# Kernel tuning notes

Measured on AMD Instinct MI355X. Metric: run time of the kernel, lower is better.

## Reference

```python
import jax, jax.numpy as jnp
import numpy as np

EPS = 1e-5


def setup_inputs() -> dict:
    key = jax.random.key(0)
    k_x, k_y, k_w, k_b = jax.random.split(key, 4)
    B, IN, OUT = 16384, 1024, 1024
    x = jax.random.normal(k_x, (B, IN), dtype=jnp.float32)
    y = jax.random.normal(k_y, (B, OUT), dtype=jnp.float32)
    # nn.Linear default init scale ~ 1/sqrt(in_features); keep activations sane
    weight = jax.random.normal(k_w, (OUT, IN), dtype=jnp.float32) / np.sqrt(IN)
    bias = jax.random.normal(k_b, (OUT,), dtype=jnp.float32) / np.sqrt(IN)
    gamma = jnp.ones((OUT,), dtype=jnp.float32)
    beta = jnp.zeros((OUT,), dtype=jnp.float32)
    return {"x": x, "y": y, "weight": weight, "bias": bias, "gamma": gamma, "beta": beta}


def reference(x, y, weight, bias, gamma, beta):
    # Linear: z[b, o] = sum_i x[b, i] * weight[o, i] + bias[o]
    z = jnp.einsum('bi,oi->bo', x, weight) + bias
    # LayerNorm over the feature (out_features) dim, biased variance
    mean = jnp.mean(z, axis=-1, keepdims=True)
    var = jnp.mean(jnp.square(z), axis=-1, keepdims=True) - jnp.square(mean)
    ln = (z - mean) * jax.lax.rsqrt(var + EPS) * gamma + beta
    # residual add then elementwise multiply
    return (ln + y) * y
```

## Files before the change

### kernel.cpp

```cpp
#include <hip/hip_runtime.h>
#include <stdint.h>

typedef unsigned short u16;
typedef __attribute__((ext_vector_type(8))) short short8;
typedef __attribute__((ext_vector_type(4))) float floatx4;
typedef __attribute__((ext_vector_type(2))) float floatx2;

#define K_DIM 1024
#define N_DIM 1024
#define BM 64
#define BK 32
#define NCHUNK (K_DIM / BK)

__device__ __forceinline__ u16 f2b(float f) {
    union { float f; uint32_t i; } v; v.f = f;
    uint32_t u = v.i;
    return (u16)((u + 0x7FFFu + ((u >> 16) & 1u)) >> 16);
}
__device__ __forceinline__ float b2f(u16 u) {
    union { uint32_t i; float f; } v; v.i = ((uint32_t)u) << 16; return v.f;
}

__global__ __launch_bounds__(256) void pack_w_kernel(const float* __restrict__ w,
                                                     u16* __restrict__ wpk) {
    int gid  = blockIdx.x * 256 + threadIdx.x;
    int lane = gid & 63;
    int kc   = (gid >> 6) & 31;
    int tile = gid >> 11;
    int n = tile * 16 + (lane & 15);
    int k = kc * 32 + (lane >> 4) * 8;
    const float* src = w + (size_t)n * K_DIM + k;
    floatx4 a = *(const floatx4*)(src);
    floatx4 b = *(const floatx4*)(src + 4);
    short8 o;
    o[0] = (short)f2b(a[0]); o[1] = (short)f2b(a[1]);
    o[2] = (short)f2b(a[2]); o[3] = (short)f2b(a[3]);
    o[4] = (short)f2b(b[0]); o[5] = (short)f2b(b[1]);
    o[6] = (short)f2b(b[2]); o[7] = (short)f2b(b[3]);
    *(short8*)(wpk + (size_t)gid * 8) = o;
}

__global__ __launch_bounds__(1024) void fused_gemm_ln_kernel(
    const float* __restrict__ x, const float* __restrict__ y,
    const u16* __restrict__ wpk, const float* __restrict__ bias,
    const float* __restrict__ gamma, const float* __restrict__ beta,
    float* __restrict__ out)
{
    __shared__ __align__(16) u16 lds_a[2][BM * BK];
    __shared__ __align__(16) u16 zbuf[16 * 1024];
    __shared__ float ls_sum[64];
    __shared__ float ls_sum2[64];
    __shared__ float ls_mean[64];
    __shared__ float ls_rs[64];

    const int tid  = threadIdx.x;
    const int lane = tid & 63;
    const int wv   = tid >> 6;
    const int q    = lane >> 4;
    const int row0 = blockIdx.x * BM;

    if (tid < 64) { ls_sum[tid] = 0.0f; ls_sum2[tid] = 0.0f; }

    const int sr = tid >> 4;
    const int sk = (tid & 15) << 1;
    const float* s_src = x + (size_t)(row0 + sr) * K_DIM + sk;
    const int s_qs  = (sk >> 3) ^ ((sr >> 1) & 3);
    const int s_off = sr * 64 + s_qs * 16 + (sk & 7) * 2;

    const u16* bp = wpk + (size_t)wv * 65536 + lane * 8;

    const int a_base = (lane & 15) * 64 + (q ^ (((lane & 15) >> 1) & 3)) * 16;

    floatx4 acc[4][4];
#pragma unroll
    for (int mi = 0; mi < 4; ++mi)
#pragma unroll
        for (int ni = 0; ni < 4; ++ni)
            acc[mi][ni] = (floatx4){0.0f, 0.0f, 0.0f, 0.0f};

    {
        floatx2 v0 = *(const floatx2*)(s_src);
        uint32_t p = (uint32_t)f2b(v0[0]) | ((uint32_t)f2b(v0[1]) << 16);
        *(uint32_t*)((char*)(&lds_a[0][0]) + s_off) = p;
    }
    floatx2 va_next = *(const floatx2*)(s_src + BK);
    floatx2 va_far  = *(const floatx2*)(s_src + 2 * BK);

    short8 bfr[2][4];
#pragma unroll
    for (int ni = 0; ni < 4; ++ni)
        bfr[0][ni] = *(const short8*)(bp + ni * 16384);
#pragma unroll
    for (int ni = 0; ni < 4; ++ni)
        bfr[1][ni] = *(const short8*)(bp + ni * 16384 + 512);

#pragma unroll 2
    for (int kc = 0; kc < NCHUNK; ++kc) {
        const int cur = kc & 1;
        const int nxt = cur ^ 1;

        asm volatile("s_waitcnt lgkmcnt(0)" ::: "memory");
        __builtin_amdgcn_s_barrier();
        asm volatile("" ::: "memory");

        short8 afrag[4];
        const char* ab = (const char*)(&lds_a[cur][0]);
#pragma unroll
        for (int mi = 0; mi < 4; ++mi)
            afrag[mi] = *(const short8*)(ab + a_base + mi * 1024);

        floatx2 vnew = (floatx2){0.0f, 0.0f};
        if (kc + 3 < NCHUNK) vnew = *(const floatx2*)(s_src + (kc + 3) * BK);

#pragma unroll
        for (int mi = 0; mi < 4; ++mi)
#pragma unroll
            for (int ni = 0; ni < 4; ++ni)
                acc[mi][ni] = __builtin_amdgcn_mfma_f32_16x16x32_bf16(
                    afrag[mi], bfr[cur][ni], acc[mi][ni], 0, 0, 0);

        if (kc + 2 < NCHUNK) {
#pragma unroll
            for (int ni = 0; ni < 4; ++ni)
                bfr[cur][ni] = *(const short8*)(bp + ni * 16384 + (kc + 2) * 512);
        }

        if (kc + 1 < NCHUNK) {
            uint32_t p = (uint32_t)f2b(va_next[0]) | ((uint32_t)f2b(va_next[1]) << 16);
            *(uint32_t*)((char*)(&lds_a[nxt][0]) + s_off) = p;
            va_next = va_far;
            va_far  = vnew;
        }
    }

    float bias_v[4];
#pragma unroll
    for (int ni = 0; ni < 4; ++ni)
        bias_v[ni] = bias[(wv << 6) + (ni << 4) + (lane & 15)];
#pragma unroll
    for (int mi = 0; mi < 4; ++mi)
#pragma unroll
        for (int ni = 0; ni < 4; ++ni)
#pragma unroll
            for (int r = 0; r < 4; ++r)
                acc[mi][ni][r] += bias_v[ni];

#pragma unroll
    for (int mi = 0; mi < 4; ++mi)
#pragma unroll
        for (int r = 0; r < 4; ++r) {
            float s = 0.0f, s2 = 0.0f;
#pragma unroll
            for (int ni = 0; ni < 4; ++ni) {
                float v = acc[mi][ni][r];
                s += v; s2 += v * v;
            }
#pragma unroll
            for (int m = 1; m < 16; m <<= 1) {
                s  += __shfl_xor(s,  m, 64);
                s2 += __shfl_xor(s2, m, 64);
            }
            if ((lane & 15) == 0) {
                int rl = (mi << 4) + (q << 2) + r;
                atomicAdd(&ls_sum[rl], s);
                atomicAdd(&ls_sum2[rl], s2);
            }
        }

    __syncthreads();
    if (tid < 64) {
        float mean = ls_sum[tid] * (1.0f / 1024.0f);
        float var  = ls_sum2[tid] * (1.0f / 1024.0f) - mean * mean;
        ls_mean[tid] = mean;
        ls_rs[tid]   = rsqrtf(var + 1e-5f);
    }

    for (int mi = 0; mi < 4; ++mi) {
#pragma unroll
        for (int ni = 0; ni < 4; ++ni)
#pragma unroll
            for (int r = 0; r < 4; ++r) {
                int lr   = (q << 2) + r;
                int lin  = (((wv << 6) + (ni << 4) + (lane & 15)) << 1);
                int phys = lr * 2048 + (lin ^ (q << 5));
                *(u16*)((char*)zbuf + phys) = f2b(acc[mi][ni][r]);
            }
        __syncthreads();
#pragma unroll
        for (int it = 0; it < 2; ++it) {
            int row  = (tid >> 7) + (it << 3);
            int c8   = tid & 127;
            int phys = row * 2048 + ((c8 << 4) ^ (((row >> 2) & 3) << 5));
            short8 z8 = *(const short8*)((const char*)zbuf + phys);
            int grow  = row0 + (mi << 4) + row;
            float mean = ls_mean[(mi << 4) + row];
            float rs   = ls_rs[(mi << 4) + row];
            const float* yp = y     + (size_t)grow * N_DIM + c8 * 8;
            const float* gp = gamma + c8 * 8;
            const float* bpv = beta + c8 * 8;
            float*       op = out   + (size_t)grow * N_DIM + c8 * 8;
            floatx4 y0 = *(const floatx4*)(yp);
            floatx4 y1 = *(const floatx4*)(yp + 4);
            floatx4 g0 = *(const floatx4*)(gp);
            floatx4 g1 = *(const floatx4*)(gp + 4);
            floatx4 b0 = *(const floatx4*)(bpv);
            floatx4 b1 = *(const floatx4*)(bpv + 4);
            floatx4 o0, o1;
#pragma unroll
            for (int e = 0; e < 4; ++e) {
                float zv = b2f((u16)z8[e]);
                o0[e] = ((zv - mean) * rs * g0[e] + b0[e] + y0[e]) * y0[e];
            }
#pragma unroll
            for (int e = 0; e < 4; ++e) {
                float zv = b2f((u16)z8[e + 4]);
                o1[e] = ((zv - mean) * rs * g1[e] + b1[e] + y1[e]) * y1[e];
            }
            *(floatx4*)(op)     = o0;
            *(floatx4*)(op + 4) = o1;
        }
        __syncthreads();
    }
}

extern "C" void kernel_launch(void* const* d_in, const int* in_sizes, int n_in,
                              void* d_out, int out_size, void* d_ws, size_t ws_size,
                              hipStream_t stream) {
    const float* x     = (const float*)d_in[0];
    const float* y     = (const float*)d_in[1];
    const float* wgt   = (const float*)d_in[2];
    const float* bias  = (const float*)d_in[3];
    const float* gamma = (const float*)d_in[4];
    const float* beta  = (const float*)d_in[5];
    float* out = (float*)d_out;
    u16* wpk = (u16*)d_ws;

    pack_w_kernel<<<512, 256, 0, stream>>>(wgt, wpk);

    const int M = in_sizes[0] / K_DIM;
    fused_gemm_ln_kernel<<<M / BM, 1024, 0, stream>>>(x, y, wpk, bias, gamma, beta, out);
}
```

Measured before the change: 225.2 us.

## Split GEMM main loop into two barrier-separated MFMA phases with priority raising

Splits each K-chunk iteration into two halves. Each half loads two A fragments and two B fragments for the next chunk, then runs its MFMAs at raised wave priority (s_setprio). Global B loads are now prefetched one chunk ahead instead of two, and the bf16 store of the next A tile is placed between the phases. The aim is to interleave memory traffic with matrix-core work, at the cost of four workgroup barriers per iteration instead of one and a shorter prefetch distance for B.

Result: faster. 217.9 us (-3.2%).

```diff
diff --git a/kernel.cpp b/kernel.cpp
--- a/kernel.cpp
+++ b/kernel.cpp
@@ -90,47 +90,59 @@
 #pragma unroll
     for (int ni = 0; ni < 4; ++ni)
         bfr[0][ni] = *(const short8*)(bp + ni * 16384);
-#pragma unroll
-    for (int ni = 0; ni < 4; ++ni)
-        bfr[1][ni] = *(const short8*)(bp + ni * 16384 + 512);
+
+    __syncthreads();
 
 #pragma unroll 2
     for (int kc = 0; kc < NCHUNK; ++kc) {
         const int cur = kc & 1;
         const int nxt = cur ^ 1;
-
+        const char* ab = (const char*)(&lds_a[cur][0]);
+        const int kn = (kc + 1 < NCHUNK) ? (kc + 1) : kc;
+
+        short8 af0 = *(const short8*)(ab + a_base);
+        short8 af1 = *(const short8*)(ab + a_base + 1024);
+        bfr[nxt][0] = *(const short8*)(bp + 0 * 16384 + kn * 512);
+        bfr[nxt][1] = *(const short8*)(bp + 1 * 16384 + kn * 512);
+        const int ka = (kc + 3 < NCHUNK) ? (kc + 3) : (NCHUNK - 1);
+        floatx2 vnew = *(const floatx2*)(s_src + ka * BK);
+
+        __builtin_amdgcn_s_barrier();
         asm volatile("s_waitcnt lgkmcnt(0)" ::: "memory");
-        __builtin_amdgcn_s_barrier();
-        asm volatile("" ::: "memory");
-
-        short8 afrag[4];
-        const char* ab = (const char*)(&lds_a[cur][0]);
-#pragma unroll
-        for (int mi = 0; mi < 4; ++mi)
-            afrag[mi] = *(const short8*)(ab + a_base + mi * 1024);
-
-        floatx2 vnew = (floatx2){0.0f, 0.0f};
-        if (kc + 3 < NCHUNK) vnew = *(const floatx2*)(s_src + (kc + 3) * BK);
-
-#pragma unroll
-        for (int mi = 0; mi < 4; ++mi)
-#pragma unroll
-            for (int ni = 0; ni < 4; ++ni)
-                acc[mi][ni] = __builtin_amdgcn_mfma_f32_16x16x32_bf16(
-                    afrag[mi], bfr[cur][ni], acc[mi][ni], 0, 0, 0);
-
-        if (kc + 2 < NCHUNK) {
-#pragma unroll
-            for (int ni = 0; ni < 4; ++ni)
-                bfr[cur][ni] = *(const short8*)(bp + ni * 16384 + (kc + 2) * 512);
-        }
-
-        if (kc + 1 < NCHUNK) {
+        __builtin_amdgcn_s_setprio(1);
+#pragma unroll
+        for (int ni = 0; ni < 4; ++ni) {
+            acc[0][ni] = __builtin_amdgcn_mfma_f32_16x16x32_bf16(
+                af0, bfr[cur][ni], acc[0][ni], 0, 0, 0);
+            acc[1][ni] = __builtin_amdgcn_mfma_f32_16x16x32_bf16(
+                af1, bfr[cur][ni], acc[1][ni], 0, 0, 0);
+        }
+        __builtin_amdgcn_s_setprio(0);
+        __builtin_amdgcn_s_barrier();
+
+        short8 af2 = *(const short8*)(ab + a_base + 2048);
+        short8 af3 = *(const short8*)(ab + a_base + 3072);
+        bfr[nxt][2] = *(const short8*)(bp + 2 * 16384 + kn * 512);
+        bfr[nxt][3] = *(const short8*)(bp + 3 * 16384 + kn * 512);
+        {
             uint32_t p = (uint32_t)f2b(va_next[0]) | ((uint32_t)f2b(va_next[1]) << 16);
             *(uint32_t*)((char*)(&lds_a[nxt][0]) + s_off) = p;
             va_next = va_far;
             va_far  = vnew;
         }
+
+        __builtin_amdgcn_s_barrier();
+        asm volatile("s_waitcnt lgkmcnt(0)" ::: "memory");
+        __builtin_amdgcn_s_setprio(1);
+#pragma unroll
+        for (int ni = 0; ni < 4; ++ni) {
+            acc[2][ni] = __builtin_amdgcn_mfma_f32_16x16x32_bf16(
+                af2, bfr[cur][ni], acc[2][ni], 0, 0, 0);
+            acc[3][ni] = __builtin_amdgcn_mfma_f32_16x16x32_bf16(
+                af3, bfr[cur][ni], acc[3][ni], 0, 0, 0);
+        }
+        __builtin_amdgcn_s_setprio(0);
+        __builtin_amdgcn_s_barrier();
     }
 
     float bias_v[4];
```
